# Optimization experiments

Measured on AMD Instinct MI355X. Metric: run time of the kernel, lower is better.

Reference implementation:

```python
import math
import jax, jax.numpy as jnp
import numpy as np

B, L, DIM, H = 2, 2048, 1024, 16
HD = DIM // H  # 64
EPS = 1e-6


def _rms_norm(x):
    # x: [..., d] float32; no learned weight (trainable=False)
    norm = jax.lax.rsqrt(jnp.mean(jnp.square(x), axis=-1, keepdims=True) + EPS)
    return x * norm


def _apply_rotary(x, cos, sin):
    # x: [b, h, l, d]; cos/sin: [1, 1, l, d//2]
    d = x.shape[-1] // 2
    x1, x2 = x[..., :d], x[..., d:]
    y1 = x1 * cos + x2 * sin
    y2 = -x1 * sin + x2 * cos
    return jnp.concatenate([y1, y2], axis=-1)


def setup_inputs() -> dict:
    key = jax.random.key(0)
    ks = jax.random.split(key, 6)
    s = 0.02
    return {
        "x": jax.random.normal(ks[0], (B, L, DIM), dtype=jnp.float32),
        "v_0": jax.random.normal(ks[1], (B, H, L, HD), dtype=jnp.float32),
        "rope_cos": jnp.cos(jax.random.normal(ks[2], (1, 1, L, HD // 2), dtype=jnp.float32)),
        "rope_sin": jnp.sin(jax.random.normal(ks[2], (1, 1, L, HD // 2), dtype=jnp.float32)),
        "qkv_w": jax.random.normal(ks[3], (3 * DIM, DIM), dtype=jnp.float32) * s,
        "proj_w": jax.random.normal(ks[4], (DIM, DIM), dtype=jnp.float32) * s,
        "lambda_param": jnp.full((1,), 0.5, dtype=jnp.float32),
    }


def reference(x, v_0, rope_cos, rope_sin, qkv_w, proj_w, lambda_param):
    b, l, dim = x.shape
    # QKV projection (no bias): [b, l, 3*dim]
    qkv = jnp.einsum('bld,ed->ble', x, qkv_w)
    # rearrange 'b l (k h d) -> k b h l d'
    qkv = qkv.reshape(b, l, 3, H, HD).transpose(2, 0, 3, 1, 4)
    q, k, v = qkv[0], qkv[1], qkv[2]
    # residual-v blend
    lam = lambda_param.reshape(())
    v = lam * v + (1.0 - lam) * v_0
    # RoPE (done in float32, inputs already float32)
    q = _apply_rotary(q, rope_cos, rope_sin)
    k = _apply_rotary(k, rope_cos, rope_sin)
    # dynamic softmax temperature
    ratio = math.sqrt(math.log(l) / math.log(1040.0))
    k = k * ratio
    # QKNorm (RMSNorm over head_dim, no weight)
    q = _rms_norm(q)
    k = _rms_norm(k)
    # scaled dot product attention
    scale = 1.0 / math.sqrt(HD)
    scores = jnp.einsum('bhqd,bhkd->bhqk', q, k) * scale
    attn = jax.nn.softmax(scores, axis=-1)
    out = jnp.einsum('bhqk,bhkd->bhqd', attn, v)
    # 'b h l d -> b l (h d)' then output projection (no bias)
    out = out.transpose(0, 2, 1, 3).reshape(b, l, dim)
    out = jnp.einsum('bld,ed->ble', out, proj_w)
    return (out, v)
```

## Files before the change

### kernel.cpp

```cpp
#include <hip/hip_runtime.h>

typedef _Float16 f16;
typedef _Float16 f16x8 __attribute__((ext_vector_type(8)));
typedef _Float16 f16x4 __attribute__((ext_vector_type(4)));
typedef float f32x4 __attribute__((ext_vector_type(4)));

#define MFMA32(a, b, c) __builtin_amdgcn_mfma_f32_16x16x32_f16((a), (b), (c), 0, 0, 0)

constexpr int Bs = 2, Ls = 2048, DIM = 1024, NH = 16, HD = 64;
constexpr int BL = Bs * Ls;
constexpr float EPSV = 1e-6f;
constexpr float SCL2 = 0.125f * 1.44269504f;

__device__ __forceinline__ float fexp2(float x) {
#if __has_builtin(__builtin_amdgcn_exp2f)
  return __builtin_amdgcn_exp2f(x);
#else
  return exp2f(x);
#endif
}

__device__ __forceinline__ int sw32(int r, int q) {
  int p = r >> 1;
  return p * 64 + ((((r & 1) * 4 + q) ^ (p & 7)) * 8);
}

__global__ void cvt_all_kernel(const float* __restrict__ x, const float* __restrict__ wq,
                               const float* __restrict__ wp, f16* __restrict__ xf,
                               f16* __restrict__ wqf, f16* __restrict__ wpf) {
  constexpr int NX4 = BL * DIM / 4;
  constexpr int NW4 = 3 * DIM * DIM / 4;
  int i = blockIdx.x * blockDim.x + threadIdx.x;
  const f32x4* src;
  f16x4* dst;
  int j;
  if (i < NX4) {
    src = (const f32x4*)x; dst = (f16x4*)xf; j = i;
  } else if (i < NX4 + NW4) {
    src = (const f32x4*)wq; dst = (f16x4*)wqf; j = i - NX4;
  } else {
    src = (const f32x4*)wp; dst = (f16x4*)wpf; j = i - NX4 - NW4;
  }
  f32x4 a = __builtin_nontemporal_load(&src[j]);
  f16x4 o = {(f16)a[0], (f16)a[1], (f16)a[2], (f16)a[3]};
  dst[j] = o;
}

__global__ __launch_bounds__(256) void qkv_gemm_kernel(
    const f16* __restrict__ A, const f16* __restrict__ W,
    const float* __restrict__ v0,
    const float* __restrict__ rcos, const float* __restrict__ rsin,
    const float* __restrict__ lamp,
    f16* __restrict__ qb, f16* __restrict__ kb, f16* __restrict__ vbT,
    float* __restrict__ vout) {
  constexpr int K = DIM;
  __shared__ alignas(16) f16 sm[4][128 * 32];
  const int tid = threadIdx.x;
  const int w = tid >> 6, lane = tid & 63, ln = lane & 15, quad = lane >> 4;
  const int wm = w >> 1, wn = w & 1;
  const int m0 = blockIdx.y * 128, n0 = blockIdx.x * 128;

  const f16* gA[2];
  const f16* gB[2];
#pragma unroll
  for (int s = 0; s < 2; ++s) {
    int lc = tid + s * 256;
    int p = lc >> 3, g = (lc & 7) ^ (p & 7);
    int r = 2 * p + (g >> 2), ce = (g & 3) * 8;
    gA[s] = A + (size_t)(m0 + r) * K + ce;
    gB[s] = W + (size_t)(n0 + r) * K + ce;
  }

  f16x8 rA[3][2], rB[3][2];
  auto loadT = [&](int k0, int pr) {
#pragma unroll
    for (int s = 0; s < 2; ++s) {
      rA[pr][s] = *(const f16x8*)(gA[s] + k0);
      rB[pr][s] = *(const f16x8*)(gB[s] + k0);
    }
  };
  auto writeT = [&](int buf, int pr) {
#pragma unroll
    for (int s = 0; s < 2; ++s) {
      *(f16x8*)&sm[buf][(tid + s * 256) * 8] = rA[pr][s];
      *(f16x8*)&sm[2 + buf][(tid + s * 256) * 8] = rB[pr][s];
    }
  };

  f32x4 acc[4][4] = {};

  loadT(0, 0);
  loadT(32, 1);
  loadT(64, 2);
  writeT(0, 0);
  __syncthreads();

#pragma unroll
  for (int it = 0; it < 32; ++it) {
    const int cur = it & 1, nxt = cur ^ 1;
    if (it < 29) loadT((it + 3) * 32, (it + 3) % 3);
    f16x8 a[4];
#pragma unroll
    for (int mi = 0; mi < 4; ++mi)
      a[mi] = *(const f16x8*)&sm[cur][sw32(wm * 64 + mi * 16 + ln, quad)];
#pragma unroll
    for (int ni = 0; ni < 4; ++ni) {
      f16x8 b = *(const f16x8*)&sm[2 + cur][sw32(wn * 64 + ni * 16 + ln, quad)];
#pragma unroll
      for (int mi = 0; mi < 4; ++mi) acc[mi][ni] = MFMA32(a[mi], b, acc[mi][ni]);
    }
    if (it < 31) writeT(nxt, (it + 1) % 3);
    __syncthreads();
  }

  const int nb = n0 + wn * 64;
  const int nsec = nb >> 10;
  const int h = (nb & 1023) >> 6;

  if (nsec == 2) {
    const float lam = lamp[0];
    const int l064 = m0 + wm * 64;
    const int b = l064 >> 11, l0 = l064 & 2047;
    const size_t vb = (size_t)(b * NH + h) * Ls * HD;
    f16* wT = &sm[0][0] + w * 4096;
#pragma unroll
    for (int mi = 0; mi < 4; ++mi) {
#pragma unroll
      for (int ni = 0; ni < 4; ++ni) {
        const int d = ni * 16 + ln;
        f16 pk[4];
#pragma unroll
        for (int rg = 0; rg < 4; ++rg) {
          const int kk = mi * 16 + quad * 4 + rg;
          const size_t base = vb + (size_t)(l0 + kk) * HD + d;
          float vnew = lam * acc[mi][ni][rg] + (1.0f - lam) * v0[base];
          vout[base] = vnew;
          pk[rg] = (f16)vnew;
        }
        f16x4 q4 = {pk[0], pk[1], pk[2], pk[3]};
        const int sidx0 = quad * 16 + mi * 4;
        *(f16x4*)&wT[d * 64 + (sidx0 ^ ((d & 7) << 3))] = q4;
      }
    }
    const size_t tB = (size_t)(b * NH + h) * HD * Ls + l0;
#pragma unroll
    for (int dd = 0; dd < 16; ++dd) {
      const int d = dd * 4 + quad;
      f16x4 vv = *(const f16x4*)&wT[d * 64 + ((ln * 4) ^ ((d & 7) << 3))];
      *(f16x4*)&vbT[tB + (size_t)d * Ls + ln * 4] = vv;
    }
  } else {
    f16* dst = nsec ? kb : qb;
    const float ratio = sqrtf(logf(2048.0f) / logf(1040.0f));
    const float post = nsec ? 1.0f : SCL2;
#pragma unroll
    for (int mi = 0; mi < 4; ++mi) {
#pragma unroll
      for (int rg = 0; rg < 4; ++rg) {
        int row = m0 + wm * 64 + mi * 16 + quad * 4 + rg;
        int b = row >> 11, l = row & 2047;
        float vals[4];
#pragma unroll
        for (int ni = 0; ni < 4; ++ni) vals[ni] = acc[mi][ni][rg];
#pragma unroll
        for (int t = 0; t < 2; ++t) {
          int j = t * 16 + ln;
          float c = rcos[l * 32 + j], s = rsin[l * 32 + j];
          float x1 = vals[t], x2 = vals[t + 2];
          vals[t] = x1 * c + x2 * s;
          vals[t + 2] = -x1 * s + x2 * c;
        }
        if (nsec) {
#pragma unroll
          for (int ni = 0; ni < 4; ++ni) vals[ni] *= ratio;
        }
        float ms = vals[0] * vals[0] + vals[1] * vals[1] + vals[2] * vals[2] + vals[3] * vals[3];
        ms += __shfl_xor(ms, 1);
        ms += __shfl_xor(ms, 2);
        ms += __shfl_xor(ms, 4);
        ms += __shfl_xor(ms, 8);
        float rn = rsqrtf(ms * (1.0f / 64.0f) + EPSV) * post;
        size_t base = ((size_t)(b * NH + h) * Ls + l) * HD;
#pragma unroll
        for (int ni = 0; ni < 4; ++ni) dst[base + ni * 16 + ln] = (f16)(vals[ni] * rn);
      }
    }
  }
}

__global__ __launch_bounds__(512, 4) void flash_kernel(
    const f16* __restrict__ qg, const f16* __restrict__ kg, const f16* __restrict__ vtg,
    f16* __restrict__ ao) {
  __shared__ alignas(16) f16 sK[2][2][64 * 64];
  __shared__ alignas(16) f16 sVT[2][2][64 * 64];
  const int tid = threadIdx.x;
  const int w = tid >> 6, lane = tid & 63, ln = lane & 15, quad = lane >> 4;
  const int grp = w >> 2, wl = w & 3;
  const int gt = tid & 255;
  const int bx = blockIdx.x;
  const int bh = bx & 31, qt = bx >> 5;
  const int h = bh & 15, b = bh >> 4;
  const f16* Qh = qg + (size_t)(b * NH + h) * Ls * HD;
  const f16* Kh = kg + (size_t)(b * NH + h) * Ls * HD;
  const f16* VTh = vtg + (size_t)(b * NH + h) * HD * Ls;
  const int q0 = qt * 128;

  f16x8 aq[2][2];
#pragma unroll
  for (int st = 0; st < 2; ++st)
#pragma unroll
    for (int kk = 0; kk < 2; ++kk)
      aq[st][kk] = *(const f16x8*)&Qh[(size_t)(q0 + wl * 32 + st * 16 + ln) * HD + kk * 32 + quad * 8];

  f16x8 kr[2], vr[2];
  auto loadKV = [&](int k0) {
#pragma unroll
    for (int s = 0; s < 2; ++s) {
      int ch = gt + s * 256, r = ch >> 3, cg = (ch & 7) * 8;
      kr[s] = *(const f16x8*)&Kh[(size_t)(k0 + r) * HD + cg];
      vr[s] = *(const f16x8*)&VTh[(size_t)r * Ls + k0 + cg];
    }
  };
  auto stageKV = [&](int buf) {
#pragma unroll
    for (int s = 0; s < 2; ++s) {
      int ch = gt + s * 256, r = ch >> 3;
      int po = r * 64 + (((ch & 7) ^ (r & 7)) * 8);
      *(f16x8*)&sK[grp][buf][po] = kr[s];
      *(f16x8*)&sVT[grp][buf][po] = vr[s];
    }
  };

  f32x4 O[2][4] = {};
  f32x4 racc[2] = {};
  const f16x8 onesv = {(f16)1.f, (f16)1.f, (f16)1.f, (f16)1.f,
                       (f16)1.f, (f16)1.f, (f16)1.f, (f16)1.f};
  const f32x4 zc = {};

  const int kbase = grp << 10;
  loadKV(kbase);
  stageKV(0);
  __syncthreads();

#pragma unroll 2
  for (int t = 0; t < 16; ++t) {
    const int cur = t & 1;
    if (t < 15) loadKV(kbase + (t + 1) * 64);

    f16x8 pA[2][2];
#pragma unroll
    for (int nt = 0; nt < 4; ++nt) {
      const int r = nt * 16 + ln;
      const f16x8 kf0 = *(const f16x8*)&sK[grp][cur][r * 64 + ((quad ^ (r & 7)) * 8)];
      const f16x8 kf1 = *(const f16x8*)&sK[grp][cur][r * 64 + (((4 + quad) ^ (r & 7)) * 8)];
#pragma unroll
      for (int st = 0; st < 2; ++st) {
        f32x4 z = MFMA32(kf1, aq[st][1], MFMA32(kf0, aq[st][0], zc));
#pragma unroll
        for (int j = 0; j < 4; ++j)
          pA[st][nt >> 1][(nt & 1) * 4 + j] = (f16)fexp2(z[j]);
      }
    }

    __builtin_amdgcn_s_setprio(1);
#pragma unroll
    for (int st = 0; st < 2; ++st) {
      racc[st] = MFMA32(pA[st][0], onesv, racc[st]);
      racc[st] = MFMA32(pA[st][1], onesv, racc[st]);
    }
#pragma unroll
    for (int dt = 0; dt < 4; ++dt) {
      const int row = dt * 16 + ln;
#pragma unroll
      for (int nt2 = 0; nt2 < 2; ++nt2) {
        const f16x8 vf = *(const f16x8*)&sVT[grp][cur][row * 64 + (((quad * 2 + nt2) ^ (row & 7)) * 8)];
#pragma unroll
        for (int st = 0; st < 2; ++st)
          O[st][dt] = MFMA32(pA[st][nt2], vf, O[st][dt]);
      }
    }
    __builtin_amdgcn_s_setprio(0);

    if (t < 15) stageKV(cur ^ 1);
    __syncthreads();
  }

  float* cO = (float*)&sK[0][0][0];
  float* cR = (float*)&sVT[0][0][0];
  if (grp == 1) {
#pragma unroll
    for (int st = 0; st < 2; ++st) {
#pragma unroll
      for (int rg = 0; rg < 4; ++rg) {
        const int ql = wl * 32 + st * 16 + quad * 4 + rg;
#pragma unroll
        for (int dt = 0; dt < 4; ++dt) cO[ql * 64 + dt * 16 + ln] = O[st][dt][rg];
        if (ln == 0) cR[ql] = racc[st][rg];
      }
    }
  }
  __syncthreads();
  if (grp == 0) {
#pragma unroll
    for (int st = 0; st < 2; ++st) {
#pragma unroll
      for (int rg = 0; rg < 4; ++rg) {
        const int ql = wl * 32 + st * 16 + quad * 4 + rg;
        const float inv = 1.0f / (racc[st][rg] + cR[ql]);
        const int q = q0 + ql;
        const size_t orow = ((size_t)b * Ls + q) * DIM + h * HD;
#pragma unroll
        for (int dt = 0; dt < 4; ++dt)
          ao[orow + dt * 16 + ln] = (f16)((O[st][dt][rg] + cO[ql * 64 + dt * 16 + ln]) * inv);
      }
    }
  }
}

__global__ __launch_bounds__(256) void proj_gemm_kernel(
    const f16* __restrict__ A, const f16* __restrict__ W, float* __restrict__ out) {
  constexpr int K = DIM;
  __shared__ alignas(16) f16 sA[2][64 * 32];
  __shared__ alignas(16) f16 sB[2][128 * 32];
  const int tid = threadIdx.x;
  const int w = tid >> 6, lane = tid & 63, ln = lane & 15, quad = lane >> 4;
  const int wm = w >> 1, wn = w & 1;
  const int m0 = blockIdx.y * 64, n0 = blockIdx.x * 128;

  const f16* gA;
  {
    int p = tid >> 3, g = (tid & 7) ^ (p & 7);
    gA = A + (size_t)(m0 + 2 * p + (g >> 2)) * K + (g & 3) * 8;
  }
  const f16* gB[2];
#pragma unroll
  for (int s = 0; s < 2; ++s) {
    int lc = tid + s * 256;
    int p = lc >> 3, g = (lc & 7) ^ (p & 7);
    gB[s] = W + (size_t)(n0 + 2 * p + (g >> 2)) * K + (g & 3) * 8;
  }

  f16x8 rA[3], rB[3][2];
  auto loadT = [&](int k0, int pr) {
    rA[pr] = *(const f16x8*)(gA + k0);
#pragma unroll
    for (int s = 0; s < 2; ++s) rB[pr][s] = *(const f16x8*)(gB[s] + k0);
  };
  auto writeT = [&](int buf, int pr) {
    *(f16x8*)&sA[buf][tid * 8] = rA[pr];
#pragma unroll
    for (int s = 0; s < 2; ++s) *(f16x8*)&sB[buf][(tid + s * 256) * 8] = rB[pr][s];
  };

  f32x4 acc[2][4] = {};

  loadT(0, 0);
  loadT(32, 1);
  loadT(64, 2);
  writeT(0, 0);
  __syncthreads();

#pragma unroll
  for (int it = 0; it < 32; ++it) {
    const int cur = it & 1, nxt = cur ^ 1;
    if (it < 29) loadT((it + 3) * 32, (it + 3) % 3);
    f16x8 a[2];
#pragma unroll
    for (int mi = 0; mi < 2; ++mi)
      a[mi] = *(const f16x8*)&sA[cur][sw32(wm * 32 + mi * 16 + ln, quad)];
#pragma unroll
    for (int ni = 0; ni < 4; ++ni) {
      f16x8 b = *(const f16x8*)&sB[cur][sw32(wn * 64 + ni * 16 + ln, quad)];
#pragma unroll
      for (int mi = 0; mi < 2; ++mi) acc[mi][ni] = MFMA32(a[mi], b, acc[mi][ni]);
    }
    if (it < 31) writeT(nxt, (it + 1) % 3);
    __syncthreads();
  }

#pragma unroll
  for (int mi = 0; mi < 2; ++mi) {
#pragma unroll
    for (int rg = 0; rg < 4; ++rg) {
      int row = m0 + wm * 32 + mi * 16 + quad * 4 + rg;
      size_t o = (size_t)row * DIM + n0 + wn * 64;
#pragma unroll
      for (int ni = 0; ni < 4; ++ni) out[o + ni * 16 + ln] = acc[mi][ni][rg];
    }
  }
}

extern "C" void kernel_launch(void* const* d_in, const int* in_sizes, int n_in,
                              void* d_out, int out_size, void* d_ws, size_t ws_size,
                              hipStream_t stream) {
  (void)in_sizes; (void)n_in; (void)out_size; (void)ws_size;
  const float* x = (const float*)d_in[0];
  const float* v0 = (const float*)d_in[1];
  const float* rcos = (const float*)d_in[2];
  const float* rsin = (const float*)d_in[3];
  const float* wqkv = (const float*)d_in[4];
  const float* wproj = (const float*)d_in[5];
  const float* lamp = (const float*)d_in[6];
  float* out = (float*)d_out;
  float* vout = out + (size_t)BL * DIM;

  char* p = (char*)d_ws;
  auto take = [&](size_t n) { char* q = p; p += ((n + 255) / 256) * 256; return q; };
  f16* xf = (f16*)take((size_t)BL * DIM * 2);
  f16* wqf = (f16*)take((size_t)3 * DIM * DIM * 2);
  f16* wpf = (f16*)take((size_t)DIM * DIM * 2);
  f16* qb = (f16*)take((size_t)BL * DIM * 2);
  f16* kb = (f16*)take((size_t)BL * DIM * 2);
  f16* vbT = (f16*)take((size_t)BL * DIM * 2);
  f16* ao = xf;

  constexpr int NCVT4 = (BL * DIM + 3 * DIM * DIM + DIM * DIM) / 4;
  cvt_all_kernel<<<dim3(NCVT4 / 256), dim3(256), 0, stream>>>(x, wqkv, wproj, xf, wqf, wpf);

  qkv_gemm_kernel<<<dim3(3 * DIM / 128, BL / 128), dim3(256), 0, stream>>>(
      xf, wqf, v0, rcos, rsin, lamp, qb, kb, vbT, vout);

  flash_kernel<<<dim3(Bs * NH * (Ls / 128)), dim3(512), 0, stream>>>(qb, kb, vbT, ao);

  proj_gemm_kernel<<<dim3(DIM / 128, BL / 64), dim3(256), 0, stream>>>(ao, wpf, out);
}
```

Baseline: 201.4 us.

## Shrink QKV GEMM tile to 128x64 with double-buffered prefetch and higher occupancy

The QKV projection GEMM moves from 128x128 block tiles to 128x64, so each block covers exactly one head along N and each of the four waves owns a 32-row strip. The register prefetch depth drops from three stages to two, and launch bounds ask for five blocks per CU. The aim is to double the grid (768 blocks) and raise occupancy on the many-CU GPU. The cost is less operand reuse per block, more A-tile traffic, and an extra barrier in the V-transpose epilogue because pairs of waves now share a transpose buffer.

```diff
diff --git a/kernel.cpp b/kernel.cpp
--- a/kernel.cpp
+++ b/kernel.cpp
@@ -46,7 +46,7 @@
   dst[j] = o;
 }
 
-__global__ __launch_bounds__(256) void qkv_gemm_kernel(
+__global__ __launch_bounds__(256, 5) void qkv_gemm_kernel(
     const f16* __restrict__ A, const f16* __restrict__ W,
     const float* __restrict__ v0,
     const float* __restrict__ rcos, const float* __restrict__ rsin,
@@ -54,98 +54,95 @@
     f16* __restrict__ qb, f16* __restrict__ kb, f16* __restrict__ vbT,
     float* __restrict__ vout) {
   constexpr int K = DIM;
-  __shared__ alignas(16) f16 sm[4][128 * 32];
+  __shared__ alignas(16) f16 sA[2][128 * 32];
+  __shared__ alignas(16) f16 sB[2][64 * 32];
   const int tid = threadIdx.x;
   const int w = tid >> 6, lane = tid & 63, ln = lane & 15, quad = lane >> 4;
-  const int wm = w >> 1, wn = w & 1;
-  const int m0 = blockIdx.y * 128, n0 = blockIdx.x * 128;
+  const int m0 = blockIdx.y * 128, n0 = blockIdx.x * 64;
 
   const f16* gA[2];
-  const f16* gB[2];
+  const f16* gB;
 #pragma unroll
   for (int s = 0; s < 2; ++s) {
     int lc = tid + s * 256;
     int p = lc >> 3, g = (lc & 7) ^ (p & 7);
-    int r = 2 * p + (g >> 2), ce = (g & 3) * 8;
-    gA[s] = A + (size_t)(m0 + r) * K + ce;
-    gB[s] = W + (size_t)(n0 + r) * K + ce;
-  }
-
-  f16x8 rA[3][2], rB[3][2];
+    gA[s] = A + (size_t)(m0 + 2 * p + (g >> 2)) * K + (g & 3) * 8;
+  }
+  {
+    int p = tid >> 3, g = (tid & 7) ^ (p & 7);
+    gB = W + (size_t)(n0 + 2 * p + (g >> 2)) * K + (g & 3) * 8;
+  }
+
+  f16x8 rA[2][2], rB[2];
   auto loadT = [&](int k0, int pr) {
 #pragma unroll
-    for (int s = 0; s < 2; ++s) {
-      rA[pr][s] = *(const f16x8*)(gA[s] + k0);
-      rB[pr][s] = *(const f16x8*)(gB[s] + k0);
-    }
+    for (int s = 0; s < 2; ++s) rA[pr][s] = *(const f16x8*)(gA[s] + k0);
+    rB[pr] = *(const f16x8*)(gB + k0);
   };
   auto writeT = [&](int buf, int pr) {
 #pragma unroll
-    for (int s = 0; s < 2; ++s) {
-      *(f16x8*)&sm[buf][(tid + s * 256) * 8] = rA[pr][s];
-      *(f16x8*)&sm[2 + buf][(tid + s * 256) * 8] = rB[pr][s];
-    }
-  };
-
-  f32x4 acc[4][4] = {};
+    for (int s = 0; s < 2; ++s) *(f16x8*)&sA[buf][(tid + s * 256) * 8] = rA[pr][s];
+    *(f16x8*)&sB[buf][tid * 8] = rB[pr];
+  };
+
+  f32x4 acc[2][4] = {};
 
   loadT(0, 0);
   loadT(32, 1);
-  loadT(64, 2);
   writeT(0, 0);
   __syncthreads();
 
 #pragma unroll
   for (int it = 0; it < 32; ++it) {
     const int cur = it & 1, nxt = cur ^ 1;
-    if (it < 29) loadT((it + 3) * 32, (it + 3) % 3);
-    f16x8 a[4];
-#pragma unroll
-    for (int mi = 0; mi < 4; ++mi)
-      a[mi] = *(const f16x8*)&sm[cur][sw32(wm * 64 + mi * 16 + ln, quad)];
+    if (it < 30) loadT((it + 2) * 32, cur);
+    f16x8 a[2];
+#pragma unroll
+    for (int mi = 0; mi < 2; ++mi)
+      a[mi] = *(const f16x8*)&sA[cur][sw32(w * 32 + mi * 16 + ln, quad)];
 #pragma unroll
     for (int ni = 0; ni < 4; ++ni) {
-      f16x8 b = *(const f16x8*)&sm[2 + cur][sw32(wn * 64 + ni * 16 + ln, quad)];
-#pragma unroll
-      for (int mi = 0; mi < 4; ++mi) acc[mi][ni] = MFMA32(a[mi], b, acc[mi][ni]);
-    }
-    if (it < 31) writeT(nxt, (it + 1) % 3);
+      f16x8 b = *(const f16x8*)&sB[cur][sw32(ni * 16 + ln, quad)];
+#pragma unroll
+      for (int mi = 0; mi < 2; ++mi) acc[mi][ni] = MFMA32(a[mi], b, acc[mi][ni]);
+    }
+    if (it < 31) writeT(nxt, nxt);
     __syncthreads();
   }
 
-  const int nb = n0 + wn * 64;
-  const int nsec = nb >> 10;
-  const int h = (nb & 1023) >> 6;
+  const int nsec = n0 >> 10;
+  const int h = (n0 & 1023) >> 6;
 
   if (nsec == 2) {
     const float lam = lamp[0];
-    const int l064 = m0 + wm * 64;
-    const int b = l064 >> 11, l0 = l064 & 2047;
+    const int prow = m0 + (w >> 1) * 64;
+    const int b = prow >> 11, l0 = prow & 2047;
     const size_t vb = (size_t)(b * NH + h) * Ls * HD;
-    f16* wT = &sm[0][0] + w * 4096;
-#pragma unroll
-    for (int mi = 0; mi < 4; ++mi) {
+    f16* wT = &sA[0][0] + (w >> 1) * 4096;
+#pragma unroll
+    for (int mi = 0; mi < 2; ++mi) {
 #pragma unroll
       for (int ni = 0; ni < 4; ++ni) {
         const int d = ni * 16 + ln;
         f16 pk[4];
 #pragma unroll
         for (int rg = 0; rg < 4; ++rg) {
-          const int kk = mi * 16 + quad * 4 + rg;
+          const int kk = (w & 1) * 32 + mi * 16 + quad * 4 + rg;
           const size_t base = vb + (size_t)(l0 + kk) * HD + d;
           float vnew = lam * acc[mi][ni][rg] + (1.0f - lam) * v0[base];
           vout[base] = vnew;
           pk[rg] = (f16)vnew;
         }
         f16x4 q4 = {pk[0], pk[1], pk[2], pk[3]};
-        const int sidx0 = quad * 16 + mi * 4;
+        const int sidx0 = quad * 16 + (mi + 2 * (w & 1)) * 4;
         *(f16x4*)&wT[d * 64 + (sidx0 ^ ((d & 7) << 3))] = q4;
       }
     }
+    __syncthreads();
     const size_t tB = (size_t)(b * NH + h) * HD * Ls + l0;
 #pragma unroll
-    for (int dd = 0; dd < 16; ++dd) {
-      const int d = dd * 4 + quad;
+    for (int dd = 0; dd < 8; ++dd) {
+      const int d = (w & 1) * 32 + dd * 4 + quad;
       f16x4 vv = *(const f16x4*)&wT[d * 64 + ((ln * 4) ^ ((d & 7) << 3))];
       *(f16x4*)&vbT[tB + (size_t)d * Ls + ln * 4] = vv;
     }
@@ -154,10 +151,10 @@
     const float ratio = sqrtf(logf(2048.0f) / logf(1040.0f));
     const float post = nsec ? 1.0f : SCL2;
 #pragma unroll
-    for (int mi = 0; mi < 4; ++mi) {
+    for (int mi = 0; mi < 2; ++mi) {
 #pragma unroll
       for (int rg = 0; rg < 4; ++rg) {
-        int row = m0 + wm * 64 + mi * 16 + quad * 4 + rg;
+        int row = m0 + w * 32 + mi * 16 + quad * 4 + rg;
         int b = row >> 11, l = row & 2047;
         float vals[4];
 #pragma unroll
@@ -417,7 +414,7 @@
   constexpr int NCVT4 = (BL * DIM + 3 * DIM * DIM + DIM * DIM) / 4;
   cvt_all_kernel<<<dim3(NCVT4 / 256), dim3(256), 0, stream>>>(x, wqkv, wproj, xf, wqf, wpf);
 
-  qkv_gemm_kernel<<<dim3(3 * DIM / 128, BL / 128), dim3(256), 0, stream>>>(
+  qkv_gemm_kernel<<<dim3(3 * DIM / 64, BL / 128), dim3(256), 0, stream>>>(
       xf, wqf, v0, rcos, rsin, lamp, qb, kb, vbT, vout);
 
   flash_kernel<<<dim3(Bs * NH * (Ls / 128)), dim3(512), 0, stream>>>(qb, kb, vbT, ao);
```

After: 200.5 us. About the same (-0.4%).
